# Performance work log

Hardware: AMD Instinct MI355X
Metric: run time of the kernel (lower is better)

Reference implementation:

```python
import jax, jax.numpy as jnp
import numpy as np

NG, ND, CIN = 100000, 50000, 128
H, D = 8, 32
HID = H * D
E = 200000
SCALE = 1.0 / np.sqrt(D)


def _segment_softmax(logits, seg, num):
    # logits: [E, H]; softmax over edges sharing the same destination node
    m = jax.ops.segment_max(logits, seg, num_segments=num)
    m = jnp.where(jnp.isfinite(m), m, 0.0)  # guard empty segments
    e = jnp.exp(logits - m[seg])
    s = jax.ops.segment_sum(e, seg, num_segments=num)
    return e / (s[seg] + 1e-16)


def _kqv(x, Wk, bk, Wq, bq, Wv, bv):
    n = x.shape[0]
    return ((x @ Wk + bk).reshape(n, H, D),
            (x @ Wq + bq).reshape(n, H, D),
            (x @ Wv + bv).reshape(n, H, D))


def _message(k_src, v_src, q_dst, src, dst, a_rel, m_rel, p_rel, n_dst):
    # per-edge-type relation transform of gathered K/V, softmax over dst, scatter-add
    k_e = jnp.einsum('ehd,hdf->ehf', k_src[src], a_rel)          # [E,H,D]
    v_e = jnp.einsum('ehd,hdf->ehf', v_src[src], m_rel)          # [E,H,D]
    logits = jnp.einsum('ehf,ehf->eh', q_dst[dst], k_e) * p_rel * SCALE
    alpha = _segment_softmax(logits, dst, n_dst)                 # [E,H]
    return jax.ops.segment_sum(alpha[..., None] * v_e, dst, num_segments=n_dst)


def _forward(x_gene, x_disease, Win_g, bin_g, Wk_g, bk_g, Wq_g, bq_g, Wv_g, bv_g,
             Wa_g, ba_g, skip_g, Win_d, bin_d, Wk_d, bk_d, Wq_d, bq_d, Wv_d, bv_d,
             Wa_d, ba_d, skip_d, a_g2d, m_g2d, p_g2d, a_d2g, m_d2g, p_d2g,
             a_g2g, m_g2g, p_g2g, prelu_w,
             g2d_src, g2d_dst, d2g_src, d2g_dst, g2g_src, g2g_dst):
    # per-type input projection (Encoder.lin_dict)
    xg = x_gene @ Win_g + bin_g      # [NG, HID]
    xd = x_disease @ Win_d + bin_d   # [ND, HID]
    ng, nd = xg.shape[0], xd.shape[0]
    kg, qg, vg = _kqv(xg, Wk_g, bk_g, Wq_g, bq_g, Wv_g, bv_g)
    kd, qd, vd = _kqv(xd, Wk_d, bk_d, Wq_d, bq_d, Wv_d, bv_d)
    # HGTConv: message passing per edge type, summed per destination type
    out_d = _message(kg, vg, qd, g2d_src, g2d_dst, a_g2d, m_g2d, p_g2d, nd)
    out_g = (_message(kd, vd, qg, d2g_src, d2g_dst, a_d2g, m_d2g, p_d2g, ng)
             + _message(kg, vg, qg, g2g_src, g2g_dst, a_g2g, m_g2g, p_g2g, ng))

    def finish(out, x_proj, Wa, ba, skip):
        h = jax.nn.gelu(out.reshape(-1, HID), approximate=False) @ Wa + ba
        beta = jax.nn.sigmoid(skip)
        h = beta * h + (1.0 - beta) * x_proj          # HGT skip connection
        return jnp.where(h > 0, h, prelu_w * h)       # PReLU; Dropout=identity (eval)

    return (finish(out_g, xg, Wa_g, ba_g, skip_g),
            finish(out_d, xd, Wa_d, ba_d, skip_d))


def setup_inputs():
    key = jax.random.key(0)
    ki = iter(jax.random.split(key, 64))
    def nrm(shape, s):
        return (jax.random.normal(next(ki), shape) * s).astype(jnp.float32)
    inp = {}
    inp['x_gene'] = jax.random.normal(next(ki), (NG, CIN), jnp.float32)
    inp['x_disease'] = jax.random.normal(next(ki), (ND, CIN), jnp.float32)
    for t in ('g', 'd'):
        inp[f'Win_{t}'] = nrm((CIN, HID), 0.09)
        inp[f'bin_{t}'] = jnp.zeros((HID,), jnp.float32)
        for p in ('k', 'q', 'v'):
            inp[f'W{p}_{t}'] = nrm((HID, HID), 0.06)
            inp[f'b{p}_{t}'] = jnp.zeros((HID,), jnp.float32)
        inp[f'Wa_{t}'] = nrm((HID, HID), 0.06)
        inp[f'ba_{t}'] = jnp.zeros((HID,), jnp.float32)
        inp[f'skip_{t}'] = jnp.ones((1,), jnp.float32)
    for r in ('g2d', 'd2g', 'g2g'):
        inp[f'a_{r}'] = nrm((H, D, D), 0.18)
        inp[f'm_{r}'] = nrm((H, D, D), 0.18)
        inp[f'p_{r}'] = jnp.ones((H,), jnp.float32)
    inp['prelu_w'] = jnp.full((HID,), 0.25, jnp.float32)
    sizes = {'g2d': (NG, ND), 'd2g': (ND, NG), 'g2g': (NG, NG)}
    for r, (ns_, nd_) in sizes.items():
        inp[f'{r}_src'] = jax.random.randint(next(ki), (E,), 0, ns_, jnp.int32)
        inp[f'{r}_dst'] = jax.random.randint(next(ki), (E,), 0, nd_, jnp.int32)
    return inp


def reference(x_gene, x_disease, Win_g, bin_g, Wk_g, bk_g, Wq_g, bq_g, Wv_g, bv_g,
              Wa_g, ba_g, skip_g, Win_d, bin_d, Wk_d, bk_d, Wq_d, bq_d, Wv_d, bv_d,
              Wa_d, ba_d, skip_d, a_g2d, m_g2d, p_g2d, a_d2g, m_d2g, p_d2g,
              a_g2g, m_g2g, p_g2g, prelu_w,
              g2d_src, g2d_dst, d2g_src, d2g_dst, g2g_src, g2g_dst):
    return _forward(x_gene, x_disease, Win_g, bin_g, Wk_g, bk_g, Wq_g, bq_g, Wv_g, bv_g,
                    Wa_g, ba_g, skip_g, Win_d, bin_d, Wk_d, bk_d, Wq_d, bq_d, Wv_d, bv_d,
                    Wa_d, ba_d, skip_d, a_g2d, m_g2d, p_g2d, a_d2g, m_d2g, p_d2g,
                    a_g2g, m_g2g, p_g2g, prelu_w,
                    g2d_src, g2d_dst, d2g_src, d2g_dst, g2g_src, g2g_dst)
```

## Files before the change

### kernel.cpp

```cpp
#include <hip/hip_runtime.h>
#include <hip/hip_bf16.h>
#include <math.h>

typedef unsigned short u16;
typedef __attribute__((ext_vector_type(4))) float f32x4;
typedef __attribute__((ext_vector_type(8))) short s16x8;

__device__ __forceinline__ float b2f(u16 u){
  union { unsigned u; float f; } v; v.u = ((unsigned)u) << 16; return v.f;
}
__device__ __forceinline__ u16 f2b(float f){
  union { float f; unsigned u; } v; v.f = f;
  unsigned r = v.u + 0x7fffu + ((v.u >> 16) & 1u);
  return (u16)(r >> 16);
}

__device__ __forceinline__ void gload_lds(const u16* g, u16* l){
  __builtin_amdgcn_global_load_lds(
      (const __attribute__((address_space(1))) unsigned*)g,
      (__attribute__((address_space(3))) unsigned*)l, 16, 0, 0);
}

__device__ __forceinline__ int chunk_swz(int bid, int nwg){
  int q = nwg >> 3, r = nwg & 7;
  int xcd = bid & 7, off = bid >> 3;
  return (xcd < r ? xcd*(q+1) : r*(q+1) + (xcd-r)*q) + off;
}

__global__ void zero_k(int* __restrict__ p, int n){
  int i = blockIdx.x*256 + threadIdx.x;
  if(i < n) p[i] = 0;
}

struct T6 { const float* W[6]; u16* O[6]; int K[6]; };
__global__ void transpose6(T6 a){
  int r = blockIdx.y;
  int idx = blockIdx.x*256 + threadIdx.x;
  int K = a.K[r];
  if(idx < K*256){ int k = idx >> 8, n = idx & 255; a.O[r][n*K + k] = f2b(a.W[r][idx]); }
}

struct F6 { const float* Wk[6]; const float* A[6]; u16* O[6]; };
__global__ void foldw6(F6 fa){
  int r = blockIdx.y;
  int idx = blockIdx.x*256 + threadIdx.x;
  int n = idx >> 8, k = idx & 255;
  int h = n >> 5, f = n & 31;
  const float* Wk = fa.Wk[r]; const float* A = fa.A[r];
  float s = 0.f;
  #pragma unroll 8
  for(int d = 0; d < 32; d++)
    s += Wk[k*256 + h*32 + d] * A[h*1024 + d*32 + f];
  fa.O[r][n*256 + k] = f2b(s);
}

struct Fb6 { const float* bk[6]; const float* A[6]; float* O[6]; };
__global__ void foldb6(Fb6 fa){
  int r = blockIdx.x;
  int n = threadIdx.x;
  int h = n >> 5, f = n & 31;
  float s = 0.f;
  for(int d = 0; d < 32; d++)
    s += fa.bk[r][h*32 + d] * fa.A[r][h*1024 + d*32 + f];
  fa.O[r][n] = s;
}

struct CSR3 {
  const int* src[3]; const int* dst[3]; int n[3];
  int* cnt[3]; int* rs[3]; int* cur[3]; int* col[3]; int* tot[3];
};
__global__ void count3(CSR3 c, int E){
  int r = blockIdx.y;
  int e = blockIdx.x*256 + threadIdx.x;
  if(e < E) atomicAdd(&c.cnt[r][c.dst[r][e]], 1);
}
__global__ void alloc3(CSR3 c){
  int r = blockIdx.y;
  int i = blockIdx.x*256 + threadIdx.x;
  if(i < c.n[r]) c.rs[r][i] = atomicAdd(c.tot[r], c.cnt[r][i]);
}
__global__ void fill3(CSR3 c, int E){
  int r = blockIdx.y;
  int e = blockIdx.x*256 + threadIdx.x;
  if(e < E){
    int d = c.dst[r][e];
    int p = c.rs[r][d] + atomicAdd(&c.cur[r][d], 1);
    c.col[r][p] = c.src[r][e];
  }
}

struct GMD {
  const void* A; const u16* BT; const float* bias; void* C;
  int M, K, lda, ldc, lgy, base, epi;
};
struct GM4 { GMD g[4]; int n, nblk; };

template<int AF>
__global__ __launch_bounds__(256) void gemm_multi(GM4 P){
  __shared__ u16 sh[2][128*64];
  const int t = threadIdx.x;
  const int l = chunk_swz(blockIdx.x, P.nblk);
  int g = 0;
  #pragma unroll
  for(int i = 1; i < 4; i++) if(i < P.n && l >= P.g[i].base) g = i;
  const GMD d = P.g[g];
  const int local = l - d.base;
  const int x = local >> d.lgy;
  const int y = local & ((1 << d.lgy) - 1);
  const int m0 = x << 7, n0 = y << 7;
  const int M = d.M, K = d.K, lda = d.lda, ldc = d.ldc;
  const int w = t >> 6, lane = t & 63;
  const int wm = (w >> 1) << 6;
  const int wn = (w & 1) << 6;
  const int lr = lane & 15, lq = lane >> 4;
  const int jr = lane >> 2;
  const int sp = lane & 3;
  f32x4 acc[4][4];
  #pragma unroll
  for(int i=0;i<4;i++)
    #pragma unroll
    for(int j=0;j<4;j++) acc[i][j] = (f32x4){0.f,0.f,0.f,0.f};

  if(AF){
    u16* As = sh[0];
    u16* Bs = sh[0] + 128*32;
    for(int k0 = 0; k0 < K; k0 += 32){
      const float* Af = (const float*)d.A;
      #pragma unroll
      for(int j = 0; j < 2; j++){
        int s = t + j*256;
        int rr = s >> 2, p2 = s & 3;
        int sl = p2 ^ (rr & 3);
        int gm = m0 + rr; if(gm > M-1) gm = M-1;
        const float* gp = Af + (size_t)gm*lda + k0 + sl*8;
        float4 f0 = *(const float4*)gp;
        float4 f1 = *(const float4*)(gp + 4);
        s16x8 v;
        v[0]=(short)f2b(f0.x); v[1]=(short)f2b(f0.y); v[2]=(short)f2b(f0.z); v[3]=(short)f2b(f0.w);
        v[4]=(short)f2b(f1.x); v[5]=(short)f2b(f1.y); v[6]=(short)f2b(f1.z); v[7]=(short)f2b(f1.w);
        *(s16x8*)&As[rr*32 + p2*8] = v;
      }
      #pragma unroll
      for(int i = 0; i < 2; i++){
        int rr = w*32 + i*16 + jr;
        int sl = sp ^ (rr & 3);
        gload_lds(d.BT + (size_t)(n0 + rr)*K + k0 + sl*8, &Bs[(w*32 + i*16)*32]);
      }
      __syncthreads();
      s16x8 a[4], b[4];
      #pragma unroll
      for(int mt=0; mt<4; mt++)
        a[mt] = *(const s16x8*)&As[(wm + mt*16 + lr)*32 + ((lq ^ (lr&3)) << 3)];
      #pragma unroll
      for(int nt=0; nt<4; nt++)
        b[nt] = *(const s16x8*)&Bs[(wn + nt*16 + lr)*32 + ((lq ^ (lr&3)) << 3)];
      #pragma unroll
      for(int mt=0; mt<4; mt++)
        #pragma unroll
        for(int nt=0; nt<4; nt++)
          acc[mt][nt] = __builtin_amdgcn_mfma_f32_16x16x32_bf16(a[mt], b[nt], acc[mt][nt], 0, 0, 0);
      __syncthreads();
    }
  } else {
    const u16* Ab = (const u16*)d.A;
    auto stage = [&](int kk, int bi){
      u16* As = sh[bi];
      u16* Bs = sh[bi] + 128*32;
      #pragma unroll
      for(int i = 0; i < 2; i++){
        int rr = w*32 + i*16 + jr;
        int sl = sp ^ (rr & 3);
        int gm = m0 + rr; if(gm > M-1) gm = M-1;
        gload_lds(Ab + (size_t)gm*lda + kk + sl*8, &As[(w*32 + i*16)*32]);
      }
      #pragma unroll
      for(int i = 0; i < 2; i++){
        int rr = w*32 + i*16 + jr;
        int sl = sp ^ (rr & 3);
        gload_lds(d.BT + (size_t)(n0 + rr)*K + kk + sl*8, &Bs[(w*32 + i*16)*32]);
      }
    };
    const int nt = K >> 5;
    int cur = 0;
    stage(0, 0);
    asm volatile("s_waitcnt vmcnt(0)" ::: "memory");
    __builtin_amdgcn_s_barrier();
    __builtin_amdgcn_sched_barrier(0);
    for(int ts = 0; ts < nt; ++ts){
      if(ts + 1 < nt) stage((ts+1) << 5, cur ^ 1);
      const u16* As = sh[cur];
      const u16* Bs = sh[cur] + 128*32;
      s16x8 a[4], b[4];
      #pragma unroll
      for(int mt=0; mt<4; mt++)
        a[mt] = *(const s16x8*)&As[(wm + mt*16 + lr)*32 + ((lq ^ (lr&3)) << 3)];
      #pragma unroll
      for(int nn=0; nn<4; nn++)
        b[nn] = *(const s16x8*)&Bs[(wn + nn*16 + lr)*32 + ((lq ^ (lr&3)) << 3)];
      asm volatile("s_waitcnt lgkmcnt(0)" ::: "memory");
      __builtin_amdgcn_sched_barrier(0);
      __builtin_amdgcn_s_setprio(1);
      #pragma unroll
      for(int mt=0; mt<4; mt++)
        #pragma unroll
        for(int nn=0; nn<4; nn++)
          acc[mt][nn] = __builtin_amdgcn_mfma_f32_16x16x32_bf16(a[mt], b[nn], acc[mt][nn], 0, 0, 0);
      __builtin_amdgcn_s_setprio(0);
      asm volatile("s_waitcnt vmcnt(0)" ::: "memory");
      __builtin_amdgcn_s_barrier();
      __builtin_amdgcn_sched_barrier(0);
      cur ^= 1;
    }
  }

  if(d.epi == 1){
    float* C = (float*)d.C;
    #pragma unroll
    for(int nt=0; nt<4; nt++){
      const int col = n0 + wn + nt*16 + lr;
      const float bc = d.bias[col];
      #pragma unroll
      for(int mt=0; mt<4; mt++)
        #pragma unroll
        for(int i=0;i<4;i++){
          int row = m0 + wm + mt*16 + lq*4 + i;
          if(row < M) C[(size_t)row*ldc + col] = acc[mt][nt][i] + bc;
        }
    }
  } else {
    u16* shm = sh[0];
    u16* C = (u16*)d.C;
    #pragma unroll
    for(int p = 0; p < 2; p++){
      if((w & 1) == p){
        #pragma unroll
        for(int nt=0; nt<4; nt++){
          const int cp = nt*16 + lr;
          const float bc = d.bias[n0 + p*64 + cp];
          #pragma unroll
          for(int mt=0; mt<4; mt++)
            #pragma unroll
            for(int i=0;i<4;i++){
              int row = wm + mt*16 + lq*4 + i;
              int so = (cp >> 3) ^ (row & 7);
              shm[row*64 + so*8 + (cp & 7)] = f2b(acc[mt][nt][i] + bc);
            }
        }
      }
      __syncthreads();
      {
        int row = t >> 1, hh = t & 1;
        if(m0 + row < M){
          u16* dst = C + (size_t)(m0 + row)*ldc + n0 + p*64 + hh*32;
          #pragma unroll
          for(int j=0;j<4;j++){
            int so = (hh*4 + j) ^ (row & 7);
            *(s16x8*)(dst + j*8) = *(const s16x8*)&shm[row*64 + so*8];
          }
        }
      }
      __syncthreads();
    }
  }
}

struct GE { const u16* A; const u16* BT; const float* bias; float* C;
            const u16* X; const float* skip; const float* prelu; int M, base; };
struct GE2 { GE g[2]; int nblk; };

__global__ __launch_bounds__(256) void gemm_epi2(GE2 P){
  __shared__ u16 Abuf[2][64*32];
  __shared__ u16 Bbuf[2][256*32];
  const int t = threadIdx.x;
  const int l = chunk_swz(blockIdx.x, P.nblk);
  const int g = (l >= P.g[1].base) ? 1 : 0;
  const GE d = P.g[g];
  const int m0 = (l - d.base) << 6;
  const int M = d.M;
  const int w = t >> 6, lane = t & 63;
  const int wn = w << 6;
  const int lr = lane & 15, lq = lane >> 4;
  const int jr = lane >> 2, sp = lane & 3;
  f32x4 acc[4][4];
  #pragma unroll
  for(int i=0;i<4;i++)
    #pragma unroll
    for(int j=0;j<4;j++) acc[i][j] = (f32x4){0.f,0.f,0.f,0.f};

  auto stage = [&](int kk, int bi){
    {
      int rr = w*16 + jr;
      int sl = sp ^ (rr & 3);
      int gm = m0 + rr; if(gm > M-1) gm = M-1;
      gload_lds(d.A + (size_t)gm*512 + kk + sl*8, &Abuf[bi][(w*16)*32]);
    }
    #pragma unroll
    for(int i = 0; i < 4; i++){
      int rr = w*64 + i*16 + jr;
      int sl = sp ^ (rr & 3);
      gload_lds(d.BT + (size_t)rr*256 + kk + sl*8, &Bbuf[bi][(w*64 + i*16)*32]);
    }
  };
  int cur = 0;
  stage(0, 0);
  asm volatile("s_waitcnt vmcnt(0)" ::: "memory");
  __builtin_amdgcn_s_barrier();
  __builtin_amdgcn_sched_barrier(0);
  for(int ts = 0; ts < 8; ++ts){
    if(ts + 1 < 8) stage((ts+1) << 5, cur ^ 1);
    const u16* As = Abuf[cur];
    const u16* Bs = Bbuf[cur];
    s16x8 a[4], b[4];
    #pragma unroll
    for(int mt=0; mt<4; mt++)
      a[mt] = *(const s16x8*)&As[(mt*16 + lr)*32 + ((lq ^ (lr&3)) << 3)];
    #pragma unroll
    for(int nn=0; nn<4; nn++)
      b[nn] = *(const s16x8*)&Bs[(wn + nn*16 + lr)*32 + ((lq ^ (lr&3)) << 3)];
    asm volatile("s_waitcnt lgkmcnt(0)" ::: "memory");
    __builtin_amdgcn_sched_barrier(0);
    __builtin_amdgcn_s_setprio(1);
    #pragma unroll
    for(int mt=0; mt<4; mt++)
      #pragma unroll
      for(int nn=0; nn<4; nn++)
        acc[mt][nn] = __builtin_amdgcn_mfma_f32_16x16x32_bf16(a[mt], b[nn], acc[mt][nn], 0, 0, 0);
    __builtin_amdgcn_s_setprio(0);
    asm volatile("s_waitcnt vmcnt(0)" ::: "memory");
    __builtin_amdgcn_s_barrier();
    __builtin_amdgcn_sched_barrier(0);
    cur ^= 1;
  }

  const float beta = 1.f/(1.f + __expf(-d.skip[0]));
  #pragma unroll
  for(int nt=0; nt<4; nt++){
    const int col = wn + nt*16 + lr;
    const float bc = d.bias[col];
    const float pw = d.prelu[col];
    #pragma unroll
    for(int mt=0; mt<4; mt++){
      #pragma unroll
      for(int i=0;i<4;i++){
        int row = m0 + mt*16 + lq*4 + i;
        if(row < M){
          float v = acc[mt][nt][i] + bc;
          float xv = b2f(d.X[(size_t)row*256 + col]);
          v = beta*v + (1.f - beta)*xv;
          v = v > 0.f ? v : pw*v;
          d.C[(size_t)row*256 + col] = v;
        }
      }
    }
  }
}

template<int NREL>
__global__ __launch_bounds__(256) void message_gelu_k(
    const u16* __restrict__ KV1, const float* __restrict__ p1,
    const int* __restrict__ rs1, const int* __restrict__ cnt1, const int* __restrict__ col1,
    const u16* __restrict__ KV2, const float* __restrict__ p2,
    const int* __restrict__ rs2, const int* __restrict__ cnt2, const int* __restrict__ col2,
    float* __restrict__ Qio, int n_dst)
{
  int node = (blockIdx.x << 2) + (threadIdx.x >> 6);
  if(node >= n_dst) return;
  int lane = threadIdx.x & 63;
  float4 qv = *(const float4*)(Qio + (size_t)node*256 + (lane << 2));
  float q0=qv.x, q1=qv.y, q2=qv.z, q3=qv.w;
  float o0=0.f, o1=0.f, o2=0.f, o3=0.f;
  #pragma unroll
  for(int rel = 0; rel < NREL; rel++){
    const u16* KV = rel ? KV2 : KV1;
    const float* pr = rel ? p2 : p1;
    const int* rs = rel ? rs2 : rs1;
    const int* cn = rel ? cnt2 : cnt1;
    const int* cl = rel ? col2 : col1;
    float ps = pr[lane >> 3] * 0.17677669529663687f;
    float a0=0.f,a1=0.f,a2=0.f,a3=0.f,ss=0.f,mx=-1e30f;
    int r0 = rs[node], deg = cn[node];
    int i = 0;
    for(; i + 2 <= deg; i += 2){
      const u16* e0 = KV + (size_t)cl[r0+i]  *512 + (lane<<2);
      const u16* e1 = KV + (size_t)cl[r0+i+1]*512 + (lane<<2);
      ushort4 ka = *(const ushort4*)e0;
      ushort4 va = *(const ushort4*)(e0 + 256);
      ushort4 kb = *(const ushort4*)e1;
      ushort4 vb = *(const ushort4*)(e1 + 256);
      float da = q0*b2f(ka.x) + q1*b2f(ka.y) + q2*b2f(ka.z) + q3*b2f(ka.w);
      float db = q0*b2f(kb.x) + q1*b2f(kb.y) + q2*b2f(kb.z) + q3*b2f(kb.w);
      da += __shfl_xor(da, 1); da += __shfl_xor(da, 2); da += __shfl_xor(da, 4);
      db += __shfl_xor(db, 1); db += __shfl_xor(db, 2); db += __shfl_xor(db, 4);
      float la = da * ps, lb = db * ps;
      float nm = fmaxf(mx, fmaxf(la, lb));
      float c  = __expf(mx - nm);
      float wa = __expf(la - nm);
      float wb = __expf(lb - nm);
      mx = nm;
      ss = ss*c + wa + wb;
      a0 = a0*c + wa*b2f(va.x) + wb*b2f(vb.x);
      a1 = a1*c + wa*b2f(va.y) + wb*b2f(vb.y);
      a2 = a2*c + wa*b2f(va.z) + wb*b2f(vb.z);
      a3 = a3*c + wa*b2f(va.w) + wb*b2f(vb.w);
    }
    if(i < deg){
      const u16* e0 = KV + (size_t)cl[r0+i]*512 + (lane<<2);
      ushort4 ka = *(const ushort4*)e0;
      ushort4 va = *(const ushort4*)(e0 + 256);
      float da = q0*b2f(ka.x) + q1*b2f(ka.y) + q2*b2f(ka.z) + q3*b2f(ka.w);
      da += __shfl_xor(da, 1); da += __shfl_xor(da, 2); da += __shfl_xor(da, 4);
      float la = da * ps;
      float nm = fmaxf(mx, la);
      float c  = __expf(mx - nm);
      float wa = __expf(la - nm);
      mx = nm;
      ss = ss*c + wa;
      a0 = a0*c + wa*b2f(va.x);
      a1 = a1*c + wa*b2f(va.y);
      a2 = a2*c + wa*b2f(va.z);
      a3 = a3*c + wa*b2f(va.w);
    }
    float inv = 1.f/(ss + 1e-16f);
    o0 += a0*inv; o1 += a1*inv; o2 += a2*inv; o3 += a3*inv;
  }
  const float c = 0.70710678118654752f;
  float g0 = 0.5f*o0*(1.f + erff(o0*c));
  float g1 = 0.5f*o1*(1.f + erff(o1*c));
  float g2 = 0.5f*o2*(1.f + erff(o2*c));
  float g3 = 0.5f*o3*(1.f + erff(o3*c));
  ushort4 ov;
  ov.x = f2b(g0); ov.y = f2b(g1); ov.z = f2b(g2); ov.w = f2b(g3);
  *(ushort4*)((u16*)Qio + (size_t)node*512 + (lane << 2)) = ov;
}

extern "C" void kernel_launch(void* const* d_in, const int* in_sizes, int n_in,
                              void* d_out, int out_size, void* d_ws, size_t ws_size,
                              hipStream_t stream)
{
  (void)n_in; (void)out_size; (void)ws_size;
  #define IN_F32(i) ((const float*)d_in[i])
  #define IN_I32(i) ((const int*)d_in[i])
  const int NG = in_sizes[0] / 128;
  const int ND = in_sizes[1] / 128;
  const int E  = in_sizes[34];

  char* p = (char*)d_ws;
  auto carve = [&](size_t bytes) -> void* {
    void* q = (void*)p; p += (bytes + 255) & ~(size_t)255; return q;
  };
  u16* XG   = (u16*)carve((size_t)NG*256*2);
  u16* XD   = (u16*)carve((size_t)ND*256*2);
  u16* KVG  = (u16*)carve((size_t)NG*512*2);
  u16* KVD  = (u16*)carve((size_t)ND*512*2);
  u16* WTinG = (u16*)carve(256*128*2);
  u16* WTinD = (u16*)carve(256*128*2);
  u16* WTqG  = (u16*)carve(256*256*2);
  u16* WTqD  = (u16*)carve(256*256*2);
  u16* WTaG  = (u16*)carve(256*256*2);
  u16* WTaD  = (u16*)carve(256*256*2);
  u16* KVW[3]; for(int i=0;i<3;i++) KVW[i] = (u16*)carve(512*256*2);
  float* FBV[3]; for(int i=0;i<3;i++) FBV[i] = (float*)carve(512*4);
  const int zn = 2*(ND + 2*NG) + 8;
  int* zone = (int*)carve((size_t)zn*4);
  int* cnt0 = zone;
  int* cnt1 = cnt0 + ND;
  int* cnt2 = cnt1 + NG;
  int* cur0 = cnt2 + NG;
  int* cur1 = cur0 + ND;
  int* cur2 = cur1 + NG;
  int* tot  = cur2 + NG;
  int* rs0 = (int*)carve((size_t)ND*4);
  int* rs1 = (int*)carve((size_t)NG*4);
  int* rs2 = (int*)carve((size_t)NG*4);
  int* col0 = (int*)carve((size_t)E*4);
  int* col1 = (int*)carve((size_t)E*4);
  int* col2 = (int*)carve((size_t)E*4);

  float* QGio = (float*)d_out;
  float* QDio = (float*)d_out + (size_t)NG*256;

  {
    T6 a;
    const int wi[6] = {2,13,6,17,10,21};
    u16* wo[6] = {WTinG, WTinD, WTqG, WTqD, WTaG, WTaD};
    const int kk[6] = {128,128,256,256,256,256};
    for(int i=0;i<6;i++){ a.W[i]=IN_F32(wi[i]); a.O[i]=wo[i]; a.K[i]=kk[i]; }
    transpose6<<<dim3(256,6), 256, 0, stream>>>(a);
  }
  {
    F6 a; Fb6 b;
    const int wk[6] = {4,8,15,19,4,8};
    const int bk[6] = {5,9,16,20,5,9};
    const int am[6] = {24,25,27,28,30,31};
    for(int i=0;i<6;i++){
      a.Wk[i]=IN_F32(wk[i]); a.A[i]=IN_F32(am[i]);
      a.O[i] = KVW[i>>1] + (size_t)(i & 1)*256*256;
      b.bk[i]=IN_F32(bk[i]); b.A[i]=IN_F32(am[i]);
      b.O[i] = FBV[i>>1] + (i & 1)*256;
    }
    foldw6<<<dim3(256,6), 256, 0, stream>>>(a);
    foldb6<<<6, 256, 0, stream>>>(b);
  }
  CSR3 c;
  c.src[0]=IN_I32(34); c.dst[0]=IN_I32(35); c.n[0]=ND;
  c.src[1]=IN_I32(36); c.dst[1]=IN_I32(37); c.n[1]=NG;
  c.src[2]=IN_I32(38); c.dst[2]=IN_I32(39); c.n[2]=NG;
  c.cnt[0]=cnt0; c.cnt[1]=cnt1; c.cnt[2]=cnt2;
  c.cur[0]=cur0; c.cur[1]=cur1; c.cur[2]=cur2;
  c.rs[0]=rs0; c.rs[1]=rs1; c.rs[2]=rs2;
  c.col[0]=col0; c.col[1]=col1; c.col[2]=col2;
  c.tot[0]=tot; c.tot[1]=tot+1; c.tot[2]=tot+2;
  const int eb = (E + 255) / 256;
  const int nb = (NG + 255) / 256;
  zero_k<<<(zn + 255) / 256, 256, 0, stream>>>(zone, zn);
  count3<<<dim3(eb,3), 256, 0, stream>>>(c, E);
  alloc3<<<dim3(nb,3), 256, 0, stream>>>(c);
  fill3<<<dim3(eb,3), 256, 0, stream>>>(c, E);

  const int xg = (NG + 127)/128, xd = (ND + 127)/128;

  {
    GM4 pj{};
    pj.g[0].A = d_in[0]; pj.g[0].BT = WTinG; pj.g[0].bias = IN_F32(3);  pj.g[0].C = XG;
    pj.g[0].M = NG; pj.g[0].K = 128; pj.g[0].lda = 128; pj.g[0].ldc = 256;
    pj.g[0].lgy = 1; pj.g[0].base = 0; pj.g[0].epi = 0;
    pj.g[1].A = d_in[1]; pj.g[1].BT = WTinD; pj.g[1].bias = IN_F32(14); pj.g[1].C = XD;
    pj.g[1].M = ND; pj.g[1].K = 128; pj.g[1].lda = 128; pj.g[1].ldc = 256;
    pj.g[1].lgy = 1; pj.g[1].base = xg*2; pj.g[1].epi = 0;
    pj.n = 2; pj.nblk = xg*2 + xd*2;
    gemm_multi<1><<<pj.nblk, 256, 0, stream>>>(pj);
  }

  {
    GM4 md{};
    md.g[0].A = XD; md.g[0].BT = WTqD;   md.g[0].bias = IN_F32(18); md.g[0].C = QDio;
    md.g[0].M = ND; md.g[0].K = 256; md.g[0].lda = 256; md.g[0].ldc = 256;
    md.g[0].lgy = 1; md.g[0].base = 0; md.g[0].epi = 1;
    int b1 = xd*2;
    md.g[1].A = XG; md.g[1].BT = KVW[0]; md.g[1].bias = FBV[0]; md.g[1].C = KVG;
    md.g[1].M = NG; md.g[1].K = 256; md.g[1].lda = 256; md.g[1].ldc = 512;
    md.g[1].lgy = 2; md.g[1].base = b1; md.g[1].epi = 0;
    int b2 = b1 + xg*4;
    md.g[2].A = XG; md.g[2].BT = WTqG;   md.g[2].bias = IN_F32(7); md.g[2].C = QGio;
    md.g[2].M = NG; md.g[2].K = 256; md.g[2].lda = 256; md.g[2].ldc = 256;
    md.g[2].lgy = 1; md.g[2].base = b2; md.g[2].epi = 1;
    int b3 = b2 + xg*2;
    md.g[3].A = XD; md.g[3].BT = KVW[1]; md.g[3].bias = FBV[1]; md.g[3].C = KVD;
    md.g[3].M = ND; md.g[3].K = 256; md.g[3].lda = 256; md.g[3].ldc = 512;
    md.g[3].lgy = 2; md.g[3].base = b3; md.g[3].epi = 0;
    md.n = 4; md.nblk = b3 + xd*4;
    gemm_multi<0><<<md.nblk, 256, 0, stream>>>(md);
  }

  message_gelu_k<1><<<(ND + 3) / 4, 256, 0, stream>>>(
      KVG, IN_F32(26), rs0, cnt0, col0,
      nullptr, nullptr, nullptr, nullptr, nullptr,
      QDio, ND);

  {
    GM4 k2{};
    k2.g[0].A = XG; k2.g[0].BT = KVW[2]; k2.g[0].bias = FBV[2]; k2.g[0].C = KVG;
    k2.g[0].M = NG; k2.g[0].K = 256; k2.g[0].lda = 256; k2.g[0].ldc = 512;
    k2.g[0].lgy = 2; k2.g[0].base = 0; k2.g[0].epi = 0;
    k2.n = 1; k2.nblk = xg*4;
    gemm_multi<0><<<k2.nblk, 256, 0, stream>>>(k2);
  }

  message_gelu_k<2><<<(NG + 3) / 4, 256, 0, stream>>>(
      KVD, IN_F32(29), rs1, cnt1, col1,
      KVG, IN_F32(32), rs2, cnt2, col2,
      QGio, NG);

  {
    GE2 ep{};
    ep.g[0].A = (const u16*)QGio; ep.g[0].BT = WTaG; ep.g[0].bias = IN_F32(11);
    ep.g[0].C = QGio; ep.g[0].X = XG; ep.g[0].skip = IN_F32(12); ep.g[0].prelu = IN_F32(33);
    ep.g[0].M = NG; ep.g[0].base = 0;
    ep.g[1].A = (const u16*)QDio; ep.g[1].BT = WTaD; ep.g[1].bias = IN_F32(22);
    ep.g[1].C = QDio; ep.g[1].X = XD; ep.g[1].skip = IN_F32(23); ep.g[1].prelu = IN_F32(33);
    ep.g[1].M = ND; ep.g[1].base = (NG + 63)/64;
    ep.nblk = (NG + 63)/64 + (ND + 63)/64;
    gemm_epi2<<<ep.nblk, 256, 0, stream>>>(ep);
  }
  #undef IN_F32
  #undef IN_I32
}
```

Before: 1.018 ms.

## Fold g2g K/V GEMM into batched launch and relax GEMM pipeline waits

Adds a fifth GEMM group so the gene-to-gene K/V projection goes into a separate workspace buffer and runs in the same batched launch as the other projections, when the workspace has room. This removes a separate serial GEMM launch between the two message kernels. Both GEMM kernels now wait only for the previous tile's loads (partial vmcnt) before the barrier, so the next tile's global-to-LDS prefetch can overlap the MFMA work. The cost is extra workspace memory and a larger kernel argument struct, and the partial vmcnt counts are only correct if the compiler emits exactly the expected number of loads per stage.

```diff
diff --git a/kernel.cpp b/kernel.cpp
--- a/kernel.cpp
+++ b/kernel.cpp
@@ -93,16 +93,16 @@
   const void* A; const u16* BT; const float* bias; void* C;
   int M, K, lda, ldc, lgy, base, epi;
 };
-struct GM4 { GMD g[4]; int n, nblk; };
+struct GM5 { GMD g[5]; int n, nblk; };
 
 template<int AF>
-__global__ __launch_bounds__(256) void gemm_multi(GM4 P){
+__global__ __launch_bounds__(256) void gemm_multi(GM5 P){
   __shared__ u16 sh[2][128*64];
   const int t = threadIdx.x;
   const int l = chunk_swz(blockIdx.x, P.nblk);
   int g = 0;
   #pragma unroll
-  for(int i = 1; i < 4; i++) if(i < P.n && l >= P.g[i].base) g = i;
+  for(int i = 1; i < 5; i++) if(i < P.n && l >= P.g[i].base) g = i;
   const GMD d = P.g[g];
   const int local = l - d.base;
   const int x = local >> d.lgy;
@@ -180,14 +180,18 @@
         gload_lds(d.BT + (size_t)(n0 + rr)*K + kk + sl*8, &Bs[(w*32 + i*16)*32]);
       }
     };
-    const int nt = K >> 5;
+    const int ntile = K >> 5;
     int cur = 0;
     stage(0, 0);
-    asm volatile("s_waitcnt vmcnt(0)" ::: "memory");
-    __builtin_amdgcn_s_barrier();
-    __builtin_amdgcn_sched_barrier(0);
-    for(int ts = 0; ts < nt; ++ts){
-      if(ts + 1 < nt) stage((ts+1) << 5, cur ^ 1);
+    for(int ts = 0; ts < ntile; ++ts){
+      if(ts + 1 < ntile){
+        stage((ts+1) << 5, cur ^ 1);
+        asm volatile("s_waitcnt vmcnt(4)" ::: "memory");
+      } else {
+        asm volatile("s_waitcnt vmcnt(0)" ::: "memory");
+      }
+      __builtin_amdgcn_s_barrier();
+      __builtin_amdgcn_sched_barrier(0);
       const u16* As = sh[cur];
       const u16* Bs = sh[cur] + 128*32;
       s16x8 a[4], b[4];
@@ -206,7 +210,6 @@
         for(int nn=0; nn<4; nn++)
           acc[mt][nn] = __builtin_amdgcn_mfma_f32_16x16x32_bf16(a[mt], b[nn], acc[mt][nn], 0, 0, 0);
       __builtin_amdgcn_s_setprio(0);
-      asm volatile("s_waitcnt vmcnt(0)" ::: "memory");
       __builtin_amdgcn_s_barrier();
       __builtin_amdgcn_sched_barrier(0);
       cur ^= 1;
@@ -303,11 +306,15 @@
   };
   int cur = 0;
   stage(0, 0);
-  asm volatile("s_waitcnt vmcnt(0)" ::: "memory");
-  __builtin_amdgcn_s_barrier();
-  __builtin_amdgcn_sched_barrier(0);
   for(int ts = 0; ts < 8; ++ts){
-    if(ts + 1 < 8) stage((ts+1) << 5, cur ^ 1);
+    if(ts + 1 < 8){
+      stage((ts+1) << 5, cur ^ 1);
+      asm volatile("s_waitcnt vmcnt(5)" ::: "memory");
+    } else {
+      asm volatile("s_waitcnt vmcnt(0)" ::: "memory");
+    }
+    __builtin_amdgcn_s_barrier();
+    __builtin_amdgcn_sched_barrier(0);
     const u16* As = Abuf[cur];
     const u16* Bs = Bbuf[cur];
     s16x8 a[4], b[4];
@@ -326,7 +333,6 @@
       for(int nn=0; nn<4; nn++)
         acc[mt][nn] = __builtin_amdgcn_mfma_f32_16x16x32_bf16(a[mt], b[nn], acc[mt][nn], 0, 0, 0);
     __builtin_amdgcn_s_setprio(0);
-    asm volatile("s_waitcnt vmcnt(0)" ::: "memory");
     __builtin_amdgcn_s_barrier();
     __builtin_amdgcn_sched_barrier(0);
     cur ^= 1;
@@ -437,7 +443,7 @@
                               void* d_out, int out_size, void* d_ws, size_t ws_size,
                               hipStream_t stream)
 {
-  (void)n_in; (void)out_size; (void)ws_size;
+  (void)n_in; (void)out_size;
   #define IN_F32(i) ((const float*)d_in[i])
   #define IN_I32(i) ((const int*)d_in[i])
   const int NG = in_sizes[0] / 128;
@@ -475,6 +481,12 @@
   int* col0 = (int*)carve((size_t)E*4);
   int* col1 = (int*)carve((size_t)E*4);
   int* col2 = (int*)carve((size_t)E*4);
+  u16* KVG2 = nullptr;
+  {
+    size_t used = (size_t)(p - (char*)d_ws);
+    size_t need = (size_t)NG*512*2 + 4096;
+    if(ws_size >= used + need) KVG2 = (u16*)carve((size_t)NG*512*2);
+  }
 
   float* QGio = (float*)d_out;
   float* QDio = (float*)d_out + (size_t)NG*256;
@@ -520,7 +532,7 @@
   const int xg = (NG + 127)/128, xd = (ND + 127)/128;
 
   {
-    GM4 pj{};
+    GM5 pj{};
     pj.g[0].A = d_in[0]; pj.g[0].BT = WTinG; pj.g[0].bias = IN_F32(3);  pj.g[0].C = XG;
     pj.g[0].M = NG; pj.g[0].K = 128; pj.g[0].lda = 128; pj.g[0].ldc = 256;
     pj.g[0].lgy = 1; pj.g[0].base = 0; pj.g[0].epi = 0;
@@ -532,7 +544,7 @@
   }
 
   {
-    GM4 md{};
+    GM5 md{};
     md.g[0].A = XD; md.g[0].BT = WTqD;   md.g[0].bias = IN_F32(18); md.g[0].C = QDio;
     md.g[0].M = ND; md.g[0].K = 256; md.g[0].lda = 256; md.g[0].ldc = 256;
     md.g[0].lgy = 1; md.g[0].base = 0; md.g[0].epi = 1;
@@ -548,7 +560,15 @@
     md.g[3].A = XD; md.g[3].BT = KVW[1]; md.g[3].bias = FBV[1]; md.g[3].C = KVD;
     md.g[3].M = ND; md.g[3].K = 256; md.g[3].lda = 256; md.g[3].ldc = 512;
     md.g[3].lgy = 2; md.g[3].base = b3; md.g[3].epi = 0;
-    md.n = 4; md.nblk = b3 + xd*4;
+    int b4 = b3 + xd*4;
+    if(KVG2){
+      md.g[4].A = XG; md.g[4].BT = KVW[2]; md.g[4].bias = FBV[2]; md.g[4].C = KVG2;
+      md.g[4].M = NG; md.g[4].K = 256; md.g[4].lda = 256; md.g[4].ldc = 512;
+      md.g[4].lgy = 2; md.g[4].base = b4; md.g[4].epi = 0;
+      md.n = 5; md.nblk = b4 + xg*4;
+    } else {
+      md.n = 4; md.nblk = b4;
+    }
     gemm_multi<0><<<md.nblk, 256, 0, stream>>>(md);
   }
 
@@ -557,8 +577,8 @@
       nullptr, nullptr, nullptr, nullptr, nullptr,
       QDio, ND);
 
-  {
-    GM4 k2{};
+  if(!KVG2){
+    GM5 k2{};
     k2.g[0].A = XG; k2.g[0].BT = KVW[2]; k2.g[0].bias = FBV[2]; k2.g[0].C = KVG;
     k2.g[0].M = NG; k2.g[0].K = 256; k2.g[0].lda = 256; k2.g[0].ldc = 512;
     k2.g[0].lgy = 2; k2.g[0].base = 0; k2.g[0].epi = 0;
@@ -568,7 +588,7 @@
 
   message_gelu_k<2><<<(NG + 3) / 4, 256, 0, stream>>>(
       KVD, IN_F32(29), rs1, cnt1, col1,
-      KVG, IN_F32(32), rs2, cnt2, col2,
+      KVG2 ? KVG2 : KVG, IN_F32(32), rs2, cnt2, col2,
       QGio, NG);
 
   {
```

Measured after the change: 1.022 ms. Within noise of the previous version (+0.4%).
